# Kernel optimization log

Measured on AMD Instinct MI355X. Metric: run time of the kernel, lower is better.

Reference implementation:

```python
import jax, jax.numpy as jnp
import numpy as np
from jax import lax

# Faithful JAX translation of Laplacian_Forward_Model.forward(acc=False).
# The opaque approximate multiplier (mul_wrapper) is modeled as an exact
# multiply, under which approx_sharp and accurate_sharp produce identical
# values; the original assigns x.data = approx result (values) while grads
# flow through the accurate path, so with exact multiply the single accurate
# path (with straight-through floor) reproduces the full forward math.

LAPLACIAN = np.array([-1.0, -1.0, -1.0, -1.0, 8.0, -1.0, -1.0, -1.0, -1.0]) / 8.0


def setup_inputs() -> dict:
    key = jax.random.key(0)
    k_in, = jax.random.split(key, 1)
    B = 16384
    n_mult = 1  # len(mul_approx_func_arr)
    inp = jax.random.uniform(k_in, (B, 1, 32, 32), dtype=jnp.float32) * 255.0
    weight = jnp.asarray(np.tile(LAPLACIAN, (n_mult, 1)), dtype=jnp.float32)          # (n_mult, 9)
    weight_factor = jnp.asarray(np.tile(np.array([8.0]), (n_mult, 1)), dtype=jnp.float32)  # (n_mult, 1)
    return {"input": inp, "weight": weight, "weight_factor": weight_factor}


def _sharp(x, ker):
    # depthwise 3x3 conv, padding 1 (C=1 so plain conv)
    B = x.shape[0]
    conv = lax.conv_general_dilated(x, ker, window_strides=(1, 1),
                                    padding=((1, 1), (1, 1)),
                                    dimension_numbers=("NCHW", "OIHW", "NCHW"))
    flat = conv.reshape(B, -1)
    cmax = lax.stop_gradient(flat.max(axis=1)).reshape(B, 1, 1, 1)
    cmin = lax.stop_gradient(flat.min(axis=1)).reshape(B, 1, 1, 1)
    mod = (conv - cmin) / jnp.maximum(cmax - cmin, 1e-6) * 255.0
    sharpened = x + mod
    sflat = sharpened.reshape(B, -1)
    smax = lax.stop_gradient(sflat.max(axis=1)).reshape(B, 1, 1, 1)
    smin = lax.stop_gradient(sflat.min(axis=1)).reshape(B, 1, 1, 1)
    res = jnp.clip((sharpened - smin) / jnp.clip(smax - smin, 1e-6, 255.0) * 255.0, 0.0, 255.0)
    # result.data = floor(result.data): straight-through floor
    return res + lax.stop_gradient(jnp.floor(res) - res)


def reference(input, weight, weight_factor):
    n_mult = weight.shape[0]
    outs = []
    for ii in range(n_mult):  # small fixed loop over approx-multiplier variants
        wc = jnp.clip(weight[ii], -0.999, 0.999)            # clamp + hardtanh(-1,1)
        wf = jnp.clip(weight_factor[ii], 1.001, 254.999)    # clamp + hardtanh(1,255)
        ker = (wc * wf).reshape(1, 1, 3, 3).astype(input.dtype)
        outs.append(_sharp(input, ker))
    return jnp.stack(outs, 0)  # (n_mult, B, 1, 32, 32)
```

## Files before the change

### kernel.cpp

```cpp
#include <hip/hip_runtime.h>
#include <math.h>


#define LDS_STRIDE 35

__global__ __launch_bounds__(256) void laplacian_fwd_kernel(
    const float* __restrict__ in,
    const float* __restrict__ weight,
    const float* __restrict__ wfac,
    float* __restrict__ out)
{
    __shared__ float img[34 * LDS_STRIDE];
    __shared__ float red[8];

    const int b = blockIdx.x;
    const int t = threadIdx.x;
    const float* src = in + (size_t)b * 1024;
    float* dst = out + (size_t)b * 1024;

    const float wf = fminf(fmaxf(wfac[0], 1.001f), 254.999f);
    float k[9];
#pragma unroll
    for (int i = 0; i < 9; ++i)
        k[i] = fminf(fmaxf(weight[i], -0.999f), 0.999f) * wf;

    for (int i = t; i < 34 * LDS_STRIDE; i += 256) img[i] = 0.0f;
    __syncthreads();

    const int row  = t >> 3;
    const int col0 = (t & 7) << 2;
    const float4 x4 = *(const float4*)(src + row * 32 + col0);
    {
        float* wp = &img[(row + 1) * LDS_STRIDE + (col0 + 1)];
        wp[0] = x4.x; wp[1] = x4.y; wp[2] = x4.z; wp[3] = x4.w;
    }
    __syncthreads();

    float conv[4];
#pragma unroll
    for (int j = 0; j < 4; ++j) {
        const float* p = &img[row * LDS_STRIDE + col0 + j];
        float s;
        s  = k[0] * p[0] + k[1] * p[1] + k[2] * p[2];
        p += LDS_STRIDE;
        s += k[3] * p[0] + k[4] * p[1] + k[5] * p[2];
        p += LDS_STRIDE;
        s += k[6] * p[0] + k[7] * p[1] + k[8] * p[2];
        conv[j] = s;
    }

    const int wave = t >> 6;
    const int lane = t & 63;

    float mn = fminf(fminf(conv[0], conv[1]), fminf(conv[2], conv[3]));
    float mx = fmaxf(fmaxf(conv[0], conv[1]), fmaxf(conv[2], conv[3]));
#pragma unroll
    for (int m = 1; m < 64; m <<= 1) {
        mn = fminf(mn, __shfl_xor(mn, m, 64));
        mx = fmaxf(mx, __shfl_xor(mx, m, 64));
    }
    if (lane == 0) { red[wave] = mn; red[4 + wave] = mx; }
    __syncthreads();
    const float cmin = fminf(fminf(red[0], red[1]), fminf(red[2], red[3]));
    const float cmax = fmaxf(fmaxf(red[4], red[5]), fmaxf(red[6], red[7]));
    __syncthreads();

    const float cden = fmaxf(cmax - cmin, 1e-6f);
    const float xv[4] = {x4.x, x4.y, x4.z, x4.w};
    float sh[4];
#pragma unroll
    for (int j = 0; j < 4; ++j)
        sh[j] = xv[j] + (conv[j] - cmin) / cden * 255.0f;

    mn = fminf(fminf(sh[0], sh[1]), fminf(sh[2], sh[3]));
    mx = fmaxf(fmaxf(sh[0], sh[1]), fmaxf(sh[2], sh[3]));
#pragma unroll
    for (int m = 1; m < 64; m <<= 1) {
        mn = fminf(mn, __shfl_xor(mn, m, 64));
        mx = fmaxf(mx, __shfl_xor(mx, m, 64));
    }
    if (lane == 0) { red[wave] = mn; red[4 + wave] = mx; }
    __syncthreads();
    const float smin = fminf(fminf(red[0], red[1]), fminf(red[2], red[3]));
    const float smax = fmaxf(fmaxf(red[4], red[5]), fmaxf(red[6], red[7]));

    const float sden = fminf(fmaxf(smax - smin, 1e-6f), 255.0f);
    float4 o;
    o.x = floorf(fminf(fmaxf((sh[0] - smin) / sden * 255.0f, 0.0f), 255.0f));
    o.y = floorf(fminf(fmaxf((sh[1] - smin) / sden * 255.0f, 0.0f), 255.0f));
    o.z = floorf(fminf(fmaxf((sh[2] - smin) / sden * 255.0f, 0.0f), 255.0f));
    o.w = floorf(fminf(fmaxf((sh[3] - smin) / sden * 255.0f, 0.0f), 255.0f));
    *(float4*)(dst + row * 32 + col0) = o;
}

extern "C" void kernel_launch(void* const* d_in, const int* in_sizes, int n_in,
                              void* d_out, int out_size, void* d_ws, size_t ws_size,
                              hipStream_t stream) {
    const float* in   = (const float*)d_in[0];
    const float* w    = (const float*)d_in[1];
    const float* wfac = (const float*)d_in[2];
    float* out = (float*)d_out;
    const int B = in_sizes[0] / 1024;
    laplacian_fwd_kernel<<<B, 256, 0, stream>>>(in, w, wfac, out);
}
```

Measured before the change: 125.6 us.

## Restructure Laplacian kernel: halo-only zeroing, vector LDS I/O, swizzle reductions, fewer barriers

Moves the global load before LDS init and zeroes only the halo border instead of the whole tile. The tile stride goes to 40 with an aligned interior so each thread writes and reads the tile as float4. The reductions use ds_swizzle butterflies within 32 lanes plus separate scratch arrays, which removes one barrier and the pre-store barrier. The per-element divides are replaced by one reciprocal multiply, which can change floor results by an ulp at boundaries.

```diff
diff --git a/kernel.cpp b/kernel.cpp
--- a/kernel.cpp
+++ b/kernel.cpp
@@ -2,7 +2,20 @@
 #include <math.h>
 
 
-#define LDS_STRIDE 35
+#define S 40
+
+template <int P>
+__device__ __forceinline__ float swz(float v) {
+    return __int_as_float(__builtin_amdgcn_ds_swizzle(__float_as_int(v), P));
+}
+
+__device__ __forceinline__ void butterfly32(float& mn, float& mx) {
+    mn = fminf(mn, swz<0x041F>(mn)); mx = fmaxf(mx, swz<0x041F>(mx));
+    mn = fminf(mn, swz<0x081F>(mn)); mx = fmaxf(mx, swz<0x081F>(mx));
+    mn = fminf(mn, swz<0x101F>(mn)); mx = fmaxf(mx, swz<0x101F>(mx));
+    mn = fminf(mn, swz<0x201F>(mn)); mx = fmaxf(mx, swz<0x201F>(mx));
+    mn = fminf(mn, swz<0x401F>(mn)); mx = fmaxf(mx, swz<0x401F>(mx));
+}
 
 __global__ __launch_bounds__(256) void laplacian_fwd_kernel(
     const float* __restrict__ in,
@@ -10,13 +23,24 @@
     const float* __restrict__ wfac,
     float* __restrict__ out)
 {
-    __shared__ float img[34 * LDS_STRIDE];
-    __shared__ float red[8];
+    __shared__ float img[34 * S];
+    __shared__ float redA[16];
+    __shared__ float redB[16];
 
     const int b = blockIdx.x;
     const int t = threadIdx.x;
     const float* src = in + (size_t)b * 1024;
     float* dst = out + (size_t)b * 1024;
+
+    const int row  = t >> 3;
+    const int col0 = (t & 7) << 2;
+
+    const float4 x4 = *(const float4*)(src + row * 32 + col0);
+
+    if (t < 40)       img[t] = 0.0f;
+    else if (t < 80)  img[33 * S + (t - 40)] = 0.0f;
+    else if (t < 112) img[(t - 79) * S + 3]  = 0.0f;
+    else if (t < 144) img[(t - 111) * S + 36] = 0.0f;
 
     const float wf = fminf(fmaxf(wfac[0], 1.001f), 254.999f);
     float k[9];
@@ -24,72 +48,56 @@
     for (int i = 0; i < 9; ++i)
         k[i] = fminf(fmaxf(weight[i], -0.999f), 0.999f) * wf;
 
-    for (int i = t; i < 34 * LDS_STRIDE; i += 256) img[i] = 0.0f;
+    *(float4*)&img[(row + 1) * S + (col0 + 4)] = x4;
     __syncthreads();
 
-    const int row  = t >> 3;
-    const int col0 = (t & 7) << 2;
-    const float4 x4 = *(const float4*)(src + row * 32 + col0);
-    {
-        float* wp = &img[(row + 1) * LDS_STRIDE + (col0 + 1)];
-        wp[0] = x4.x; wp[1] = x4.y; wp[2] = x4.z; wp[3] = x4.w;
+    float conv[4] = {0.0f, 0.0f, 0.0f, 0.0f};
+#pragma unroll
+    for (int r = 0; r < 3; ++r) {
+        const float* p = &img[(row + r) * S + col0];
+        const float  l  = p[3];
+        const float4 m  = *(const float4*)(p + 4);
+        const float  rr = p[8];
+        const float k0 = k[3 * r], k1 = k[3 * r + 1], k2 = k[3 * r + 2];
+        conv[0] += k0 * l   + k1 * m.x + k2 * m.y;
+        conv[1] += k0 * m.x + k1 * m.y + k2 * m.z;
+        conv[2] += k0 * m.y + k1 * m.z + k2 * m.w;
+        conv[3] += k0 * m.z + k1 * m.w + k2 * rr;
     }
-    __syncthreads();
-
-    float conv[4];
-#pragma unroll
-    for (int j = 0; j < 4; ++j) {
-        const float* p = &img[row * LDS_STRIDE + col0 + j];
-        float s;
-        s  = k[0] * p[0] + k[1] * p[1] + k[2] * p[2];
-        p += LDS_STRIDE;
-        s += k[3] * p[0] + k[4] * p[1] + k[5] * p[2];
-        p += LDS_STRIDE;
-        s += k[6] * p[0] + k[7] * p[1] + k[8] * p[2];
-        conv[j] = s;
-    }
-
-    const int wave = t >> 6;
-    const int lane = t & 63;
 
     float mn = fminf(fminf(conv[0], conv[1]), fminf(conv[2], conv[3]));
     float mx = fmaxf(fmaxf(conv[0], conv[1]), fmaxf(conv[2], conv[3]));
-#pragma unroll
-    for (int m = 1; m < 64; m <<= 1) {
-        mn = fminf(mn, __shfl_xor(mn, m, 64));
-        mx = fmaxf(mx, __shfl_xor(mx, m, 64));
-    }
-    if (lane == 0) { red[wave] = mn; red[4 + wave] = mx; }
+    butterfly32(mn, mx);
+    if ((t & 31) == 0) { redA[t >> 5] = mn; redA[8 + (t >> 5)] = mx; }
     __syncthreads();
-    const float cmin = fminf(fminf(red[0], red[1]), fminf(red[2], red[3]));
-    const float cmax = fmaxf(fmaxf(red[4], red[5]), fmaxf(red[6], red[7]));
-    __syncthreads();
+    const float cmin = fminf(fminf(fminf(redA[0], redA[1]), fminf(redA[2], redA[3])),
+                             fminf(fminf(redA[4], redA[5]), fminf(redA[6], redA[7])));
+    const float cmax = fmaxf(fmaxf(fmaxf(redA[8], redA[9]), fmaxf(redA[10], redA[11])),
+                             fmaxf(fmaxf(redA[12], redA[13]), fmaxf(redA[14], redA[15])));
 
-    const float cden = fmaxf(cmax - cmin, 1e-6f);
+    const float inv1 = 255.0f / fmaxf(cmax - cmin, 1e-6f);
     const float xv[4] = {x4.x, x4.y, x4.z, x4.w};
     float sh[4];
 #pragma unroll
     for (int j = 0; j < 4; ++j)
-        sh[j] = xv[j] + (conv[j] - cmin) / cden * 255.0f;
+        sh[j] = xv[j] + (conv[j] - cmin) * inv1;
 
     mn = fminf(fminf(sh[0], sh[1]), fminf(sh[2], sh[3]));
     mx = fmaxf(fmaxf(sh[0], sh[1]), fmaxf(sh[2], sh[3]));
-#pragma unroll
-    for (int m = 1; m < 64; m <<= 1) {
-        mn = fminf(mn, __shfl_xor(mn, m, 64));
-        mx = fmaxf(mx, __shfl_xor(mx, m, 64));
-    }
-    if (lane == 0) { red[wave] = mn; red[4 + wave] = mx; }
+    butterfly32(mn, mx);
+    if ((t & 31) == 0) { redB[t >> 5] = mn; redB[8 + (t >> 5)] = mx; }
     __syncthreads();
-    const float smin = fminf(fminf(red[0], red[1]), fminf(red[2], red[3]));
-    const float smax = fmaxf(fmaxf(red[4], red[5]), fmaxf(red[6], red[7]));
+    const float smin = fminf(fminf(fminf(redB[0], redB[1]), fminf(redB[2], redB[3])),
+                             fminf(fminf(redB[4], redB[5]), fminf(redB[6], redB[7])));
+    const float smax = fmaxf(fmaxf(fmaxf(redB[8], redB[9]), fmaxf(redB[10], redB[11])),
+                             fmaxf(fmaxf(redB[12], redB[13]), fmaxf(redB[14], redB[15])));
 
-    const float sden = fminf(fmaxf(smax - smin, 1e-6f), 255.0f);
+    const float inv2 = 255.0f / fminf(fmaxf(smax - smin, 1e-6f), 255.0f);
     float4 o;
-    o.x = floorf(fminf(fmaxf((sh[0] - smin) / sden * 255.0f, 0.0f), 255.0f));
-    o.y = floorf(fminf(fmaxf((sh[1] - smin) / sden * 255.0f, 0.0f), 255.0f));
-    o.z = floorf(fminf(fmaxf((sh[2] - smin) / sden * 255.0f, 0.0f), 255.0f));
-    o.w = floorf(fminf(fmaxf((sh[3] - smin) / sden * 255.0f, 0.0f), 255.0f));
+    o.x = floorf(fminf(fmaxf((sh[0] - smin) * inv2, 0.0f), 255.0f));
+    o.y = floorf(fminf(fmaxf((sh[1] - smin) * inv2, 0.0f), 255.0f));
+    o.z = floorf(fminf(fmaxf((sh[2] - smin) * inv2, 0.0f), 255.0f));
+    o.w = floorf(fminf(fmaxf((sh[3] - smin) * inv2, 0.0f), 255.0f));
     *(float4*)(dst + row * 32 + col0) = o;
 }
 
```

Result: no change. 124.3 us (-1.0%).
